# Kernel tuning notes

Hardware: AMD Instinct MI355X
Metric: run time of the kernel (lower is better)

## Reference

```python
import jax, jax.numpy as jnp
import numpy as np

B, S, D, V = 32, 1024, 768, 32000


def setup_inputs() -> dict:
    key = jax.random.key(0)
    ks = jax.random.split(key, 12)
    scale = 0.02
    return {
        "tokens": jax.random.randint(ks[0], (B, S), 0, V, dtype=jnp.int32),
        "mask": jax.random.randint(ks[1], (B, S), 0, 2, dtype=jnp.int32),
        "emb": jax.random.normal(ks[2], (V, D), dtype=jnp.float32) * scale,
        "wq": jax.random.normal(ks[3], (D, D), dtype=jnp.float32) * scale,
        "wk": jax.random.normal(ks[4], (D, D), dtype=jnp.float32) * scale,
        "wv": jax.random.normal(ks[5], (D, D), dtype=jnp.float32) * scale,
        "ln_g": jnp.ones((D,), dtype=jnp.float32),
        "ln_b": jnp.zeros((D,), dtype=jnp.float32),
        "w1": jax.random.normal(ks[6], (D, D), dtype=jnp.float32) * scale,
        "b1": jnp.zeros((D,), dtype=jnp.float32),
        "wh": jax.random.normal(ks[7], (D, 2), dtype=jnp.float32) * scale,
        "bh": jnp.zeros((2,), dtype=jnp.float32),
    }


def reference(tokens, mask, emb, wq, wk, wv, ln_g, ln_b, w1, b1, wh, bh):
    # embedding lookup: [B,S,D]
    x = emb[tokens]
    q = x @ wq
    k = x @ wk
    v = x @ wv
    # unscaled attention scores: [B,S,S]
    s = jnp.einsum("bsd,btd->bst", q, k)
    # additive padding mask (mask==1 -> -1e9), broadcast over query dim
    s = s + (-1e9) * mask.astype(s.dtype)[:, None, :]
    a = jax.nn.softmax(s, axis=-1)
    o = jnp.einsum("bst,btd->bsd", a, v)
    # classify on first token
    cls = o[:, 0, :]  # [B,D]
    mu = jnp.mean(cls, axis=-1, keepdims=True)
    var = jnp.var(cls, axis=-1, keepdims=True)
    h = (cls - mu) * jax.lax.rsqrt(var + 1e-5) * ln_g + ln_b
    h = jax.nn.gelu(h @ w1 + b1, approximate=False)
    logits = h @ wh + bh  # [B,2]
    return (logits, a)
```

## Files before the change

kernel.cpp:

```cpp
#include <hip/hip_runtime.h>
#include <hip/hip_bf16.h>

#define NB 32
#define SS 1024
#define DD 768

typedef __attribute__((ext_vector_type(8))) short bf16x8;
typedef __attribute__((ext_vector_type(4))) float f32x4;

__device__ inline ushort f2bf(float f) {
    union { float f; unsigned u; } x;
    x.f = f;
    unsigned r = (x.u + 0x7fffu + ((x.u >> 16) & 1u)) >> 16;
    return (ushort)r;
}

#define GLOBAL_PTR(x) ((const __attribute__((address_space(1))) void*)(x))
#define LDS_PTR(x)    ((__attribute__((address_space(3))) void*)(x))

__global__ void k_cvt(const float* __restrict__ wq, const float* __restrict__ wk,
                      ushort* __restrict__ wqb, ushort* __restrict__ wkb) {
    const int i = (blockIdx.x * 256 + threadIdx.x) * 4;
    const float* src = blockIdx.y ? wk : wq;
    ushort* dst = blockIdx.y ? wkb : wqb;
    const float4 v = *(const float4*)(src + i);
    ushort4 o;
    o.x = f2bf(v.x); o.y = f2bf(v.y); o.z = f2bf(v.z); o.w = f2bf(v.w);
    *(ushort4*)(dst + i) = o;
}

__global__ void k_gather(const int* __restrict__ tokens, const float* __restrict__ emb,
                         ushort* __restrict__ xb) {
    int i = (blockIdx.x * 256 + threadIdx.x) * 4;
    int row = i / DD;
    int col = i - row * DD;
    int tok = tokens[row];
    const float4 v = *(const float4*)(emb + (size_t)tok * DD + col);
    ushort4 o;
    o.x = f2bf(v.x); o.y = f2bf(v.y); o.z = f2bf(v.z); o.w = f2bf(v.w);
    *(ushort4*)(xb + (size_t)row * DD + col) = o;
}

template <int MODE>
__global__ __launch_bounds__(256, 2) void k_gemm(const ushort* __restrict__ A,
                                                 const ushort* __restrict__ Bt,
                                                 ushort* __restrict__ Cb,
                                                 float* __restrict__ Cs) {
    constexpr int BK = 64;
    __shared__ ushort As[2][128 * BK];
    __shared__ ushort Bs[2][128 * BK];
    const int tid = threadIdx.x;
    const int wave = tid >> 6, lane = tid & 63;

    int bx, by;
    size_t abase, bbase;
    if (MODE == 1) {
        const int wgid = blockIdx.x;
        const int g = wgid >> 9, w = wgid & 511;
        const int b = g * 8 + (w & 7);
        const int tile = w >> 3;
        bx = tile & 7; by = tile >> 3;
        abase = (size_t)b * SS * DD + (size_t)bx * 128 * DD;
        bbase = (size_t)b * SS * DD + (size_t)by * 128 * DD;
        Cs += (size_t)b * SS * SS;
    } else {
        bx = blockIdx.x; by = blockIdx.y;
        abase = (size_t)bx * 128 * DD;
        bbase = (size_t)by * 128 * DD;
    }

    const int r = tid >> 3;
    const int cc = (tid & 7) * 8;

    auto stage = [&](int buf, int k0) {
#pragma unroll
        for (int i = 0; i < 4; i++) {
            __builtin_amdgcn_global_load_lds(GLOBAL_PTR(A + abase + (size_t)(r + i * 32) * DD + k0 + cc),
                                             LDS_PTR(&As[buf][(r + i * 32) * BK + cc]), 16, 0, 0);
            __builtin_amdgcn_global_load_lds(GLOBAL_PTR(Bt + bbase + (size_t)(r + i * 32) * DD + k0 + cc),
                                             LDS_PTR(&Bs[buf][(r + i * 32) * BK + cc]), 16, 0, 0);
        }
    };

    f32x4 acc[4][4] = {};
    const int wm = (wave >> 1) * 64, wn = (wave & 1) * 64;
    const int lr = lane & 15, lc = (lane >> 4) * 8;

    stage(0, 0);
    __syncthreads();
    int cur = 0;
#pragma unroll 1
    for (int k0 = 0; k0 < DD; k0 += BK) {
        if (k0 + BK < DD) stage(cur ^ 1, k0 + BK);
        const ushort* as = As[cur];
        const ushort* bs = Bs[cur];
#pragma unroll
        for (int kk = 0; kk < 2; kk++) {
            bf16x8 af[4], bfv[4];
#pragma unroll
            for (int m = 0; m < 4; m++)
                af[m] = *(const bf16x8*)(as + (wm + m * 16 + lr) * BK + kk * 32 + lc);
#pragma unroll
            for (int n = 0; n < 4; n++)
                bfv[n] = *(const bf16x8*)(bs + (wn + n * 16 + lr) * BK + kk * 32 + lc);
#pragma unroll
            for (int m = 0; m < 4; m++)
#pragma unroll
                for (int n = 0; n < 4; n++)
                    acc[m][n] = __builtin_amdgcn_mfma_f32_16x16x32_bf16(af[m], bfv[n], acc[m][n], 0, 0, 0);
        }
        __syncthreads();
        cur ^= 1;
    }

    const int rowbase = bx * 128 + wm + (lane >> 4) * 4;
    const int colbase = by * 128 + wn + (lane & 15);
    if (MODE == 0) {
#pragma unroll
        for (int m = 0; m < 4; m++)
#pragma unroll
            for (int n = 0; n < 4; n++)
#pragma unroll
                for (int j = 0; j < 4; j++)
                    Cb[(size_t)(rowbase + m * 16 + j) * DD + colbase + n * 16] = f2bf(acc[m][n][j]);
    } else {
#pragma unroll
        for (int m = 0; m < 4; m++)
#pragma unroll
            for (int n = 0; n < 4; n++)
#pragma unroll
                for (int j = 0; j < 4; j++)
                    Cs[(size_t)(rowbase + m * 16 + j) * SS + colbase + n * 16] = acc[m][n][j];
    }
}

__global__ __launch_bounds__(256) void k_softmax(float* __restrict__ a, const int* __restrict__ mask) {
    const int rid = blockIdx.x;
    const int b = rid >> 10, rr = rid & 1023;
    float* row = a + (size_t)b * SS * SS + (size_t)rr * SS;
    const int* mrow = mask + b * SS;
    const int t = threadIdx.x * 4;
    float4 v = *(float4*)(row + t);
    const int4 mk = *(const int4*)(mrow + t);
    float x0 = v.x + (mk.x ? -1e9f : 0.0f);
    float x1 = v.y + (mk.y ? -1e9f : 0.0f);
    float x2 = v.z + (mk.z ? -1e9f : 0.0f);
    float x3 = v.w + (mk.w ? -1e9f : 0.0f);
    float mx = fmaxf(fmaxf(x0, x1), fmaxf(x2, x3));
#pragma unroll
    for (int off = 32; off; off >>= 1) mx = fmaxf(mx, __shfl_xor(mx, off));
    __shared__ float redm[4], reds[4];
    if ((threadIdx.x & 63) == 0) redm[threadIdx.x >> 6] = mx;
    __syncthreads();
    mx = fmaxf(fmaxf(redm[0], redm[1]), fmaxf(redm[2], redm[3]));
    float e0 = expf(x0 - mx), e1 = expf(x1 - mx), e2 = expf(x2 - mx), e3 = expf(x3 - mx);
    float sm = e0 + e1 + e2 + e3;
#pragma unroll
    for (int off = 32; off; off >>= 1) sm += __shfl_xor(sm, off);
    if ((threadIdx.x & 63) == 0) reds[threadIdx.x >> 6] = sm;
    __syncthreads();
    sm = reds[0] + reds[1] + reds[2] + reds[3];
    const float inv = 1.0f / sm;
    v.x = e0 * inv; v.y = e1 * inv; v.z = e2 * inv; v.w = e3 * inv;
    *(float4*)(row + t) = v;
}

__global__ __launch_bounds__(256) void k_xbar(const float* __restrict__ a, const int* __restrict__ tokens,
                                              const float* __restrict__ emb, float* __restrict__ part) {
    const int b = blockIdx.x >> 3, c = blockIdx.x & 7;
    __shared__ float a0s[128];
    __shared__ int toks[128];
    const int tid = threadIdx.x;
    if (tid < 128) {
        a0s[tid] = a[(size_t)b * SS * SS + c * 128 + tid];
        toks[tid] = tokens[b * SS + c * 128 + tid];
    }
    __syncthreads();
    float acc0 = 0.f, acc1 = 0.f, acc2 = 0.f;
#pragma unroll 4
    for (int t = 0; t < 128; t++) {
        const float at = a0s[t];
        const float* er = emb + (size_t)toks[t] * DD;
        acc0 = fmaf(at, er[tid], acc0);
        acc1 = fmaf(at, er[tid + 256], acc1);
        acc2 = fmaf(at, er[tid + 512], acc2);
    }
    float* p = part + ((size_t)c * NB + b) * DD;
    p[tid] = acc0; p[tid + 256] = acc1; p[tid + 512] = acc2;
}

__global__ __launch_bounds__(128) void k_cls(const float* __restrict__ part, const float* __restrict__ wv,
                                             float* __restrict__ cls) {
    const int b = blockIdx.y, tid = threadIdx.x;
    const int c = blockIdx.x * 128 + tid;
    __shared__ float xb[DD];
#pragma unroll
    for (int j = 0; j < 6; j++) {
        const int k = tid + j * 128;
        float s = 0.f;
#pragma unroll
        for (int p = 0; p < 8; p++) s += part[((size_t)p * NB + b) * DD + k];
        xb[k] = s;
    }
    __syncthreads();
    float acc = 0.f;
#pragma unroll 8
    for (int k = 0; k < DD; k++) acc = fmaf(xb[k], wv[(size_t)k * DD + c], acc);
    cls[(size_t)b * DD + c] = acc;
}

__device__ inline float block_sum256(float v, float* red, int tid) {
#pragma unroll
    for (int off = 32; off; off >>= 1) v += __shfl_xor(v, off);
    __syncthreads();
    if ((tid & 63) == 0) red[tid >> 6] = v;
    __syncthreads();
    return red[0] + red[1] + red[2] + red[3];
}

__global__ __launch_bounds__(256) void k_ln(const float* __restrict__ cls, const float* __restrict__ ln_g,
                                            const float* __restrict__ ln_b, float* __restrict__ hs) {
    const int b = blockIdx.x, tid = threadIdx.x;
    __shared__ float red[4];
    float v[3];
#pragma unroll
    for (int j = 0; j < 3; j++) v[j] = cls[(size_t)b * DD + tid + j * 256];
    const float mu = block_sum256(v[0] + v[1] + v[2], red, tid) * (1.0f / DD);
    float dv = 0.f;
#pragma unroll
    for (int j = 0; j < 3; j++) { const float d = v[j] - mu; dv += d * d; }
    __syncthreads();
    const float var = block_sum256(dv, red, tid) * (1.0f / DD);
    const float sc = 1.0f / sqrtf(var + 1e-5f);
#pragma unroll
    for (int j = 0; j < 3; j++) {
        const int d = tid + j * 256;
        hs[(size_t)b * DD + d] = (v[j] - mu) * sc * ln_g[d] + ln_b[d];
    }
}

__global__ __launch_bounds__(128) void k_mlp(const float* __restrict__ hs, const float* __restrict__ w1,
                                             const float* __restrict__ b1, const float* __restrict__ wh,
                                             float* __restrict__ part_l) {
    const int b = blockIdx.y, tid = threadIdx.x;
    const int j = blockIdx.x * 128 + tid;
    __shared__ float h[DD];
#pragma unroll
    for (int q = 0; q < 6; q++) h[tid + q * 128] = hs[(size_t)b * DD + tid + q * 128];
    __syncthreads();
    float p = b1[j];
#pragma unroll 8
    for (int d = 0; d < DD; d++) p = fmaf(h[d], w1[(size_t)d * DD + j], p);
    const float g = 0.5f * p * (1.0f + erff(p * 0.70710678118654752f));
    float l0 = g * wh[j * 2 + 0];
    float l1 = g * wh[j * 2 + 1];
#pragma unroll
    for (int off = 32; off; off >>= 1) { l0 += __shfl_xor(l0, off); l1 += __shfl_xor(l1, off); }
    __shared__ float r0[2], r1[2];
    if ((tid & 63) == 0) { r0[tid >> 6] = l0; r1[tid >> 6] = l1; }
    __syncthreads();
    if (tid == 0) {
        part_l[((size_t)b * 6 + blockIdx.x) * 2 + 0] = r0[0] + r0[1];
        part_l[((size_t)b * 6 + blockIdx.x) * 2 + 1] = r1[0] + r1[1];
    }
}

__global__ __launch_bounds__(64) void k_final(const float* __restrict__ part_l, const float* __restrict__ bh,
                                              float* __restrict__ out) {
    const int b = threadIdx.x;
    if (b < NB) {
        float l0 = bh[0], l1 = bh[1];
#pragma unroll
        for (int c = 0; c < 6; c++) {
            l0 += part_l[((size_t)b * 6 + c) * 2 + 0];
            l1 += part_l[((size_t)b * 6 + c) * 2 + 1];
        }
        out[b * 2 + 0] = l0;
        out[b * 2 + 1] = l1;
    }
}

extern "C" void kernel_launch(void* const* d_in, const int* in_sizes, int n_in,
                              void* d_out, int out_size, void* d_ws, size_t ws_size,
                              hipStream_t stream) {
    const int*   tokens = (const int*)d_in[0];
    const int*   mask   = (const int*)d_in[1];
    const float* emb    = (const float*)d_in[2];
    const float* wq     = (const float*)d_in[3];
    const float* wk     = (const float*)d_in[4];
    const float* wv     = (const float*)d_in[5];
    const float* ln_g   = (const float*)d_in[6];
    const float* ln_b   = (const float*)d_in[7];
    const float* w1     = (const float*)d_in[8];
    const float* b1     = (const float*)d_in[9];
    const float* wh     = (const float*)d_in[10];
    const float* bh     = (const float*)d_in[11];
    float* out = (float*)d_out;

    char* ws = (char*)d_ws;
    const size_t XB = (size_t)NB * SS * DD * 2;
    const size_t WB = (size_t)DD * DD * 2;
    ushort* xb  = (ushort*)ws;
    ushort* yb  = (ushort*)(ws + XB);
    ushort* wqb = (ushort*)(ws + 2 * XB);
    ushort* wkb = (ushort*)(ws + 2 * XB + WB);
    ushort* Wt  = (ushort*)(ws + 2 * XB + 2 * WB);
    char*   p4  = ws + 2 * XB + 3 * WB;
    float*  part   = (float*)p4;
    float*  cls    = (float*)(p4 + 786432);
    float*  hsb    = (float*)(p4 + 786432 + 98304);
    float*  part_l = (float*)(p4 + 786432 + 2 * 98304);

    float* s_region = out + 64;

    k_cvt<<<dim3(576, 2), 256, 0, stream>>>(wq, wk, wqb, wkb);
    k_gather<<<24576, 256, 0, stream>>>(tokens, emb, xb);
    k_gemm<0><<<dim3(6, 6), 256, 0, stream>>>(wkb, wqb, Wt, nullptr);
    k_gemm<0><<<dim3(256, 6), 256, 0, stream>>>(xb, Wt, yb, nullptr);
    k_gemm<1><<<2048, 256, 0, stream>>>(yb, xb, nullptr, s_region);
    k_softmax<<<32768, 256, 0, stream>>>(s_region, mask);
    k_xbar<<<256, 256, 0, stream>>>(s_region, tokens, emb, part);
    k_cls<<<dim3(6, NB), 128, 0, stream>>>(part, wv, cls);
    k_ln<<<NB, 256, 0, stream>>>(cls, ln_g, ln_b, hsb);
    k_mlp<<<dim3(6, NB), 128, 0, stream>>>(hsb, w1, b1, wh, part_l);
    k_final<<<1, 64, 0, stream>>>(part_l, bh, out);
}
```

Baseline: 379.3 us.

## Use 256x256 tiled GEMM with swizzled LDS and interleaved prefetch for large GEMMs

Adds a 512-thread GEMM kernel with 256x256 output tiles, XOR-swizzled LDS layout to avoid bank conflicts, and prefetch of the next K-tile split into quarters interleaved with MFMA work under raised wave priority. The projection GEMM and the batched score GEMM switch to it, while the small weight-product GEMM keeps the old 128x128 kernel. Larger tiles raise data reuse per LDS load and cut global traffic, at the cost of more registers (8x4 accumulators per wave), fewer workgroups, and possible occupancy limits.

```diff
diff --git a/kernel.cpp b/kernel.cpp
--- a/kernel.cpp
+++ b/kernel.cpp
@@ -41,34 +41,17 @@
     *(ushort4*)(xb + (size_t)row * DD + col) = o;
 }
 
-template <int MODE>
-__global__ __launch_bounds__(256, 2) void k_gemm(const ushort* __restrict__ A,
-                                                 const ushort* __restrict__ Bt,
-                                                 ushort* __restrict__ Cb,
-                                                 float* __restrict__ Cs) {
+__global__ __launch_bounds__(256, 2) void k_gemm_s(const ushort* __restrict__ A,
+                                                   const ushort* __restrict__ Bt,
+                                                   ushort* __restrict__ Cb) {
     constexpr int BK = 64;
     __shared__ ushort As[2][128 * BK];
     __shared__ ushort Bs[2][128 * BK];
     const int tid = threadIdx.x;
     const int wave = tid >> 6, lane = tid & 63;
-
-    int bx, by;
-    size_t abase, bbase;
-    if (MODE == 1) {
-        const int wgid = blockIdx.x;
-        const int g = wgid >> 9, w = wgid & 511;
-        const int b = g * 8 + (w & 7);
-        const int tile = w >> 3;
-        bx = tile & 7; by = tile >> 3;
-        abase = (size_t)b * SS * DD + (size_t)bx * 128 * DD;
-        bbase = (size_t)b * SS * DD + (size_t)by * 128 * DD;
-        Cs += (size_t)b * SS * SS;
-    } else {
-        bx = blockIdx.x; by = blockIdx.y;
-        abase = (size_t)bx * 128 * DD;
-        bbase = (size_t)by * 128 * DD;
-    }
-
+    const int bx = blockIdx.x, by = blockIdx.y;
+    const size_t abase = (size_t)bx * 128 * DD;
+    const size_t bbase = (size_t)by * 128 * DD;
     const int r = tid >> 3;
     const int cc = (tid & 7) * 8;
 
@@ -112,12 +95,130 @@
         __syncthreads();
         cur ^= 1;
     }
-
     const int rowbase = bx * 128 + wm + (lane >> 4) * 4;
     const int colbase = by * 128 + wn + (lane & 15);
+#pragma unroll
+    for (int m = 0; m < 4; m++)
+#pragma unroll
+        for (int n = 0; n < 4; n++)
+#pragma unroll
+            for (int j = 0; j < 4; j++)
+                Cb[(size_t)(rowbase + m * 16 + j) * DD + colbase + n * 16] = f2bf(acc[m][n][j]);
+}
+
+#define HALF_USH (128 * 64)
+template <int MODE>
+__global__ __launch_bounds__(512, 2) void k_gemm256(const ushort* __restrict__ A,
+                                                    const ushort* __restrict__ Bt,
+                                                    ushort* __restrict__ Cb,
+                                                    float* __restrict__ Cs) {
+    __shared__ ushort As[2][2][HALF_USH];
+    __shared__ ushort Bs[2][2][HALF_USH];
+    const int tid = threadIdx.x;
+    const int wid = tid >> 6, lane = tid & 63;
+    const int wm = wid >> 2, wn = wid & 3;
+    const int la = lane & 15;
+
+    int bx, by;
+    size_t abase, bbase;
+    if (MODE == 1) {
+        const int wgid = blockIdx.x;
+        const int g = wgid >> 7, w = wgid & 127;
+        const int b = g * 8 + (w & 7);
+        const int tile = w >> 3;
+        bx = tile & 3; by = tile >> 2;
+        abase = (size_t)b * SS * DD + (size_t)bx * 256 * DD;
+        bbase = (size_t)b * SS * DD + (size_t)by * 256 * DD;
+        Cs += (size_t)b * SS * SS;
+    } else {
+        bx = blockIdx.x; by = blockIdx.y;
+        abase = (size_t)bx * 256 * DD;
+        bbase = (size_t)by * 256 * DD;
+    }
+    const ushort* Ag = A + abase;
+    const ushort* Bg = Bt + bbase;
+
+    int s_r[2], s_c[2], s_d[2];
+#pragma unroll
+    for (int l = 0; l < 2; l++) {
+        const int L = (l * 512 + tid) * 16;
+        const int r = L >> 7;
+        const int cb = L & 127;
+        s_r[l] = r;
+        s_c[l] = (cb ^ ((r & 7) << 4)) >> 1;
+        s_d[l] = L >> 1;
+    }
+
+    auto stage_half = [&](ushort* dst, const ushort* gsrc) {
+#pragma unroll
+        for (int l = 0; l < 2; l++)
+            __builtin_amdgcn_global_load_lds(GLOBAL_PTR(gsrc + (size_t)s_r[l] * DD + s_c[l]),
+                                             LDS_PTR(dst + s_d[l]), 16, 0, 0);
+    };
+
+    const int swz = (la & 7) << 4;
+    const int off_k0 = (((lane >> 4) << 4) ^ swz) >> 1;
+    const int off_k1 = ((64 | ((lane >> 4) << 4)) ^ swz) >> 1;
+
+    f32x4 acc[8][4] = {};
+
+    stage_half(&As[0][0][0], Ag);
+    stage_half(&As[0][1][0], Ag + (size_t)128 * DD);
+    stage_half(&Bs[0][0][0], Bg);
+    stage_half(&Bs[0][1][0], Bg + (size_t)128 * DD);
+    __syncthreads();
+
+#pragma unroll 1
+    for (int t = 0; t < 12; t++) {
+        const int buf = t & 1;
+        const ushort* Ah = &As[buf][wm][0];
+        const ushort* Bh = &Bs[buf][wn >> 1][0];
+        const int brow0 = (wn & 1) * 64;
+        const int kt = (t + 1) * 64;
+        bf16x8 bfv[4][2];
+#pragma unroll
+        for (int q = 0; q < 4; q++) {
+            if (q == 0) {
+#pragma unroll
+                for (int n = 0; n < 4; n++) {
+                    const int rr = brow0 + n * 16 + la;
+                    bfv[n][0] = *(const bf16x8*)(Bh + rr * 64 + off_k0);
+                    bfv[n][1] = *(const bf16x8*)(Bh + rr * 64 + off_k1);
+                }
+            }
+            bf16x8 af[2][2];
+#pragma unroll
+            for (int dm = 0; dm < 2; dm++) {
+                const int rr = (q * 2 + dm) * 16 + la;
+                af[dm][0] = *(const bf16x8*)(Ah + rr * 64 + off_k0);
+                af[dm][1] = *(const bf16x8*)(Ah + rr * 64 + off_k1);
+            }
+            if (t < 11) {
+                if (q == 0) stage_half(&As[buf ^ 1][0][0], Ag + kt);
+                if (q == 1) stage_half(&As[buf ^ 1][1][0], Ag + (size_t)128 * DD + kt);
+                if (q == 2) stage_half(&Bs[buf ^ 1][0][0], Bg + kt);
+                if (q == 3) stage_half(&Bs[buf ^ 1][1][0], Bg + (size_t)128 * DD + kt);
+            }
+            __builtin_amdgcn_s_setprio(1);
+#pragma unroll
+            for (int dm = 0; dm < 2; dm++)
+#pragma unroll
+                for (int n = 0; n < 4; n++)
+#pragma unroll
+                    for (int kk = 0; kk < 2; kk++)
+                        acc[q * 2 + dm][n] = __builtin_amdgcn_mfma_f32_16x16x32_bf16(
+                            af[dm][kk], bfv[n][kk], acc[q * 2 + dm][n], 0, 0, 0);
+            __builtin_amdgcn_s_setprio(0);
+            if (q < 3) __builtin_amdgcn_s_barrier();
+        }
+        __syncthreads();
+    }
+
+    const int rowbase = bx * 256 + wm * 128 + (lane >> 4) * 4;
+    const int colbase = by * 256 + wn * 64 + la;
     if (MODE == 0) {
 #pragma unroll
-        for (int m = 0; m < 4; m++)
+        for (int m = 0; m < 8; m++)
 #pragma unroll
             for (int n = 0; n < 4; n++)
 #pragma unroll
@@ -125,7 +226,7 @@
                     Cb[(size_t)(rowbase + m * 16 + j) * DD + colbase + n * 16] = f2bf(acc[m][n][j]);
     } else {
 #pragma unroll
-        for (int m = 0; m < 4; m++)
+        for (int m = 0; m < 8; m++)
 #pragma unroll
             for (int n = 0; n < 4; n++)
 #pragma unroll
@@ -315,9 +416,9 @@
 
     k_cvt<<<dim3(576, 2), 256, 0, stream>>>(wq, wk, wqb, wkb);
     k_gather<<<24576, 256, 0, stream>>>(tokens, emb, xb);
-    k_gemm<0><<<dim3(6, 6), 256, 0, stream>>>(wkb, wqb, Wt, nullptr);
-    k_gemm<0><<<dim3(256, 6), 256, 0, stream>>>(xb, Wt, yb, nullptr);
-    k_gemm<1><<<2048, 256, 0, stream>>>(yb, xb, nullptr, s_region);
+    k_gemm_s<<<dim3(6, 6), 256, 0, stream>>>(wkb, wqb, Wt);
+    k_gemm256<0><<<dim3(128, 3), 512, 0, stream>>>(xb, Wt, yb, nullptr);
+    k_gemm256<1><<<512, 512, 0, stream>>>(yb, xb, nullptr, s_region);
     k_softmax<<<32768, 256, 0, stream>>>(s_region, mask);
     k_xbar<<<256, 256, 0, stream>>>(s_region, tokens, emb, part);
     k_cls<<<dim3(6, NB), 128, 0, stream>>>(part, wv, cls);
```

Result: faster. 337.5 us (-11.0%).
